# Optimization experiments

Measured on AMD Instinct MI355X. Metric: run time of the kernel, lower is better.

## Reference

```python
import jax, jax.numpy as jnp
import numpy as np

N = 50000      # nodes
E = 800000     # edges
FIN = 128      # num_feature
EDIM = 16      # edge_dim
OUT = 64       # out_dim (per-head channels; concat=False averages heads)
H = 4          # heads
SCALE = 1.0 / float(np.sqrt(OUT))


def _layernorm(h, g, b):
    mu = h.mean(-1, keepdims=True)
    var = ((h - mu) ** 2).mean(-1, keepdims=True)
    return (h - mu) * jax.lax.rsqrt(var + 1e-5) * g + b


def _tconv(x, src, dst, ea, Wq, bq, Wk, bk, Wv, bv, We, Ws, bs):
    # PyG TransformerConv, concat=False, root_weight=True, eval mode (no dropout)
    n = x.shape[0]
    q = (x @ Wq + bq).reshape(n, H, OUT)[dst]   # [E,H,D] query at destination
    k = (x @ Wk + bk).reshape(n, H, OUT)[src]   # [E,H,D] key at source
    v = (x @ Wv + bv).reshape(n, H, OUT)[src]   # [E,H,D] value at source
    e = (ea @ We).reshape(-1, H, OUT)           # [E,H,D] edge embedding (no bias)
    logits = jnp.einsum('ehd,ehd->eh', q, k + e) * SCALE   # [E,H]
    # segment softmax over incoming edges of each destination node
    m = jax.lax.stop_gradient(jax.ops.segment_max(logits, dst, num_segments=n))
    a = jnp.exp(logits - m[dst])
    s = jax.ops.segment_sum(a, dst, num_segments=n)
    alpha = a / s[dst]                                     # [E,H]
    agg = jax.ops.segment_sum((v + e) * alpha[..., None], dst, num_segments=n)  # [N,H,D]
    return agg.mean(axis=1) + x @ Ws + bs      # concat=False -> head mean; + skip


def _forward(x, src, dst, ea, p1, p2, p3, g, b):
    h = x
    for p in (p1, p2, p3):
        h = jax.nn.gelu(_layernorm(_tconv(h, src, dst, ea, *p), g, b), approximate=False)
    return h


def setup_inputs() -> dict:
    key = jax.random.key(0)
    ks = iter(jax.random.split(key, 64))
    def nrm(shp, s=0.05):
        return jax.random.normal(next(ks), shp, jnp.float32) * s
    inp = {
        'x': nrm((N, FIN), 1.0),
        'edge_index': jax.random.randint(next(ks), (2, E), 0, N),
        'edge_attr': nrm((E, EDIM), 1.0),
    }
    for l, fin in ((1, FIN), (2, OUT), (3, OUT)):
        inp[f'Wq{l}'] = nrm((fin, H * OUT)); inp[f'bq{l}'] = jnp.zeros((H * OUT,), jnp.float32)
        inp[f'Wk{l}'] = nrm((fin, H * OUT)); inp[f'bk{l}'] = jnp.zeros((H * OUT,), jnp.float32)
        inp[f'Wv{l}'] = nrm((fin, H * OUT)); inp[f'bv{l}'] = jnp.zeros((H * OUT,), jnp.float32)
        inp[f'We{l}'] = nrm((EDIM, H * OUT))
        inp[f'Ws{l}'] = nrm((fin, OUT)); inp[f'bs{l}'] = jnp.zeros((OUT,), jnp.float32)
    inp['ln_g'] = jnp.ones((OUT,), jnp.float32)
    inp['ln_b'] = jnp.zeros((OUT,), jnp.float32)
    return inp


def reference(x, edge_index, edge_attr,
              Wq1, bq1, Wk1, bk1, Wv1, bv1, We1, Ws1, bs1,
              Wq2, bq2, Wk2, bk2, Wv2, bv2, We2, Ws2, bs2,
              Wq3, bq3, Wk3, bk3, Wv3, bv3, We3, Ws3, bs3,
              ln_g, ln_b):
    src, dst = edge_index[0], edge_index[1]
    p1 = (Wq1, bq1, Wk1, bk1, Wv1, bv1, We1, Ws1, bs1)
    p2 = (Wq2, bq2, Wk2, bk2, Wv2, bv2, We2, Ws2, bs2)
    p3 = (Wq3, bq3, Wk3, bk3, Wv3, bv3, We3, Ws3, bs3)
    return _forward(x, src, dst, edge_attr, p1, p2, p3, ln_g, ln_b)
```

## Files before the change

kernel.cpp:

```cpp
#include <hip/hip_runtime.h>
#include <hip/hip_bf16.h>
#include <math.h>

#define NNODES 50000
#define NEDGES 800000
#define HD     256
#define CW     384
#define NTOT   896
#define QS     0.18033688011112042f

typedef __hip_bfloat16 bf16;
typedef unsigned short u16;
typedef unsigned char  u8;
typedef unsigned int   u32;
typedef __attribute__((ext_vector_type(8))) short bf16x8;
typedef __attribute__((ext_vector_type(4))) float f32x4;
typedef __attribute__((ext_vector_type(2))) float f32x2;

__device__ __forceinline__ float lo16f(u32 u) { return __uint_as_float(u << 16); }
__device__ __forceinline__ float hi16f(u32 u) { return __uint_as_float(u & 0xFFFF0000u); }
__device__ __forceinline__ short f2s(float v) { __hip_bfloat16 h = __float2bfloat16(v); return *(short*)&h; }

template<int CTRL>
__device__ __forceinline__ float dppadd(float x) {
    int t = __builtin_amdgcn_update_dpp(0, __float_as_int(x), CTRL, 0xF, 0xF, true);
    return x + __int_as_float(t);
}

__global__ void hist_kernel(const int* __restrict__ dst, int* __restrict__ deg, int E) {
    int e = blockIdx.x * 256 + threadIdx.x;
    if (e < E) atomicAdd(&deg[dst[e]], 1);
}

__global__ void scanA(const int* __restrict__ deg, int* __restrict__ locincl,
                      int* __restrict__ blocksum, int n) {
    int tid = threadIdx.x;
    int i = blockIdx.x * 256 + tid;
    int v = (i < n) ? deg[i] : 0;
    int lane = tid & 63, w = tid >> 6;
    int s = v;
    #pragma unroll
    for (int off = 1; off < 64; off <<= 1) {
        int t = __shfl_up(s, off);
        if (lane >= off) s += t;
    }
    __shared__ int wsum[4];
    if (lane == 63) wsum[w] = s;
    __syncthreads();
    for (int ww = 0; ww < w; ww++) s += wsum[ww];
    if (i < n) locincl[i] = s;
    if (tid == 255) blocksum[blockIdx.x] = s;
}

__global__ void scanB(const int* __restrict__ blocksum, int* __restrict__ blockoff,
                      int nb, int* __restrict__ rowptr, int n) {
    int tid = threadIdx.x;
    int v = (tid < nb) ? blocksum[tid] : 0;
    int lane = tid & 63, w = tid >> 6;
    int s = v;
    #pragma unroll
    for (int off = 1; off < 64; off <<= 1) {
        int t = __shfl_up(s, off);
        if (lane >= off) s += t;
    }
    __shared__ int wsum[4];
    if (lane == 63) wsum[w] = s;
    __syncthreads();
    for (int ww = 0; ww < w; ww++) s += wsum[ww];
    if (tid < nb) blockoff[tid] = s - v;
    if (tid == 255) rowptr[n] = s;
}

__global__ void scanC(const int* __restrict__ deg, const int* __restrict__ locincl,
                      const int* __restrict__ blockoff,
                      int* __restrict__ rowptr, int* __restrict__ cursor, int n) {
    int i = blockIdx.x * 256 + threadIdx.x;
    if (i < n) {
        int ex = locincl[i] - deg[i] + blockoff[blockIdx.x];
        rowptr[i] = ex;
        cursor[i] = ex;
    }
}

__global__ void scatter_kernel(const int* __restrict__ src, const int* __restrict__ dst,
                               int* __restrict__ cursor, int2* __restrict__ csr2, int E) {
    int e = blockIdx.x * 256 + threadIdx.x;
    if (e < E) {
        int d = dst[e];
        int p = atomicAdd(&cursor[d], 1);
        csr2[p] = make_int2(src[e], e);
    }
}

__global__ void xcast(const float* __restrict__ x, u16* __restrict__ xb) {
    int i = blockIdx.x * 256 + threadIdx.x;
    const float4* p = (const float4*)(x + (size_t)i * 8);
    float4 a = p[0], b = p[1];
    union { u16 s[8]; uint4 u; } t;
    t.s[0] = (u16)f2s(a.x); t.s[1] = (u16)f2s(a.y); t.s[2] = (u16)f2s(a.z); t.s[3] = (u16)f2s(a.w);
    t.s[4] = (u16)f2s(b.x); t.s[5] = (u16)f2s(b.y); t.s[6] = (u16)f2s(b.z); t.s[7] = (u16)f2s(b.w);
    *(uint4*)(xb + (size_t)i * 8) = t.u;
}

__global__ void pack_all(const float* __restrict__ Wq, const float* __restrict__ bq,
                         const float* __restrict__ Wk, const float* __restrict__ bk,
                         const float* __restrict__ Wv, const float* __restrict__ bv,
                         const float* __restrict__ We,
                         const float* __restrict__ Ws, const float* __restrict__ bs,
                         bf16* __restrict__ Wc, float* __restrict__ b, int K) {
    int n = blockIdx.x, c = threadIdx.x;
    float v, bb;
    if (n < 256)      { v = Wq[(size_t)c * 256 + n] * QS;    bb = bq[n] * QS; }
    else if (n < 320) {
        int t = n - 256, h = t >> 4, j = t & 15;
        float s = 0.f, sb = 0.f;
        #pragma unroll 8
        for (int d = 0; d < 64; d++) {
            float wv = We[j * HD + h * 64 + d];
            s += Wq[(size_t)c * 256 + h * 64 + d] * wv;
            sb += bq[h * 64 + d] * wv;
        }
        v = s * QS; bb = sb * QS;
    }
    else if (n < 384) { v = Ws[(size_t)c * 64  + (n - 320)]; bb = bs[n - 320]; }
    else if (n < 640) { v = Wv[(size_t)c * 256 + (n - 384)]; bb = bv[n - 384]; }
    else              { v = Wk[(size_t)c * 256 + (n - 640)]; bb = bk[n - 640]; }
    Wc[(size_t)n * K + c] = __float2bfloat16(v);
    if (c == 0) b[n] = bb;
}

template<int K>
__global__ void __launch_bounds__(256) gemm_reg(
    const u16* __restrict__ A, const bf16* __restrict__ Wc, const float* __restrict__ bias,
    bf16* __restrict__ comb, bf16* __restrict__ vbuf, u8* __restrict__ k8)
{
    constexpr int KS = K / 32;
    constexpr int ITERS = 8;
    __shared__ u8 TrB[4][2560];
    int tid = threadIdx.x, w = tid >> 6, lane = tid & 63;
    int cl = lane & 15, aq = lane >> 4;
    int chunk = blockIdx.x;
    int slab = blockIdx.y * (64 * ITERS);
    int mrow = slab + w * 16 + cl;
    u8* myT = TrB[w];

    bf16x8 bfr[4][KS];
    #pragma unroll
    for (int t = 0; t < 4; t++)
        #pragma unroll
        for (int ks = 0; ks < KS; ks++)
            bfr[t][ks] = *(const bf16x8*)((const u16*)Wc +
                         (size_t)(chunk * 64 + t * 16 + cl) * K + ks * 32 + aq * 8);

    float4 bv[4];
    #pragma unroll
    for (int t = 0; t < 4; t++) bv[t] = *(const float4*)&bias[chunk * 64 + t * 16 + aq * 4];

    auto LOADA = [&](bf16x8* af, int m) {
        int rc = (m < NNODES) ? m : (NNODES - 1);
        const u16* ar = A + (size_t)rc * K + aq * 8;
        #pragma unroll
        for (int ks = 0; ks < KS; ks++) af[ks] = *(const bf16x8*)(ar + ks * 32);
    };

    bf16x8 b0[KS], b1[KS], b2[KS];
    LOADA(b0, mrow);
    LOADA(b1, mrow + 64);
    #pragma unroll
    for (int it = 0; it < ITERS; it++) {
        int m = mrow + it * 64;
        if (it + 2 < ITERS) LOADA(b2, m + 128);
        f32x4 acc[4] = {};
        #pragma unroll
        for (int t = 0; t < 4; t++)
            #pragma unroll
            for (int ks = 0; ks < KS; ks++)
                acc[t] = __builtin_amdgcn_mfma_f32_16x16x32_bf16(bfr[t][ks], b0[ks], acc[t], 0, 0, 0);

        if (chunk < 10) {
            #pragma unroll
            for (int t = 0; t < 4; t++) {
                u32 lo = (u32)(u16)f2s(acc[t][0] + bv[t].x) | ((u32)(u16)f2s(acc[t][1] + bv[t].y) << 16);
                u32 hi = (u32)(u16)f2s(acc[t][2] + bv[t].z) | ((u32)(u16)f2s(acc[t][3] + bv[t].w) << 16);
                *(uint2*)(myT + cl * 160 + t * 32 + aq * 8) = make_uint2(lo, hi);
            }
            #pragma unroll
            for (int i = 0; i < 2; i++) {
                int r = i * 8 + (lane >> 3);
                uint4 vv = *(const uint4*)(myT + r * 160 + (lane & 7) * 16);
                int gr = slab + it * 64 + w * 16 + r;
                if (gr < NNODES) {
                    u16* dst = (chunk < 6) ? (u16*)comb + (size_t)gr * CW + chunk * 64
                                           : (u16*)vbuf + (size_t)gr * 256 + (chunk - 6) * 64;
                    *(uint4*)(dst + (lane & 7) * 8) = vv;
                }
            }
        } else {
            #pragma unroll
            for (int t = 0; t < 4; t++) {
                u32 pk = __builtin_amdgcn_cvt_pk_fp8_f32(acc[t][0] + bv[t].x, acc[t][1] + bv[t].y, 0, false);
                pk = __builtin_amdgcn_cvt_pk_fp8_f32(acc[t][2] + bv[t].z, acc[t][3] + bv[t].w, pk, true);
                *(u32*)(myT + cl * 80 + (t * 4 + aq) * 4) = pk;
            }
            {
                int r = lane >> 2;
                uint4 vv = *(const uint4*)(myT + r * 80 + (lane & 3) * 16);
                int gr = slab + it * 64 + w * 16 + r;
                if (gr < NNODES)
                    *(uint4*)(k8 + (size_t)gr * 256 + (chunk - 10) * 64 + (lane & 3) * 16) = vv;
            }
        }
        #pragma unroll
        for (int ks = 0; ks < KS; ks++) { b0[ks] = b1[ks]; b1[ks] = b2[ks]; }
    }
}

__global__ void __launch_bounds__(256) node_fused(
    const int* __restrict__ rowptr, const int2* __restrict__ csr2,
    const float* __restrict__ eattr, const u16* __restrict__ comb,
    const u16* __restrict__ vbuf, const u8* __restrict__ k8,
    const float* __restrict__ We, const float* __restrict__ lng, const float* __restrict__ lnb,
    bf16* __restrict__ outB, float* __restrict__ outF)
{
    int tid = threadIdx.x, w = tid >> 6, lane = tid & 63;
    int n = blockIdx.x * 4 + w;
    int hg = lane >> 4, j16 = lane & 15, coff = 4 * lane;
    __shared__ float sAV[4][256];
    __shared__ float sAE[4][64];

    const u16* crow = comb + (size_t)n * CW;
    uint2 qv = *(const uint2*)(crow + coff);
    float qf0 = lo16f(qv.x), qf1 = hi16f(qv.x), qf2 = lo16f(qv.y), qf3 = hi16f(qv.y);
    float qwe_r = __uint_as_float((u32)crow[256 + lane] << 16);

    int e0 = __builtin_amdgcn_readfirstlane(rowptr[n]);
    int e1 = __builtin_amdgcn_readfirstlane(rowptr[n + 1]);

    float ss = 0.f, av0 = 0.f, av1 = 0.f, av2 = 0.f, av3 = 0.f, ae = 0.f;
    u32 vo = (u32)coff * 2u;
    u32 eo = (u32)j16 * 4u;

    auto EDGE = [&](int2 me) {
        u32 s   = (u32)__builtin_amdgcn_readfirstlane(me.x);
        u32 eid = (u32)__builtin_amdgcn_readfirstlane(me.y);
        const char* kp = (const char*)k8    + ((size_t)s << 8);
        const char* vp = (const char*)vbuf  + ((size_t)s << 9);
        const char* ep = (const char*)eattr + ((size_t)eid << 6);
        u32   kw = *(const u32*)  (kp + coff);
        uint2 vw = *(const uint2*)(vp + vo);
        float ea = *(const float*)(ep + eo);
        f32x2 k01 = __builtin_amdgcn_cvt_pk_f32_fp8(kw, false);
        f32x2 k23 = __builtin_amdgcn_cvt_pk_f32_fp8(kw, true);
        float part = qf0 * k01[0] + qf1 * k01[1] + qf2 * k23[0] + qf3 * k23[1] + qwe_r * ea;
        part = dppadd<0xB1>(part);
        part = dppadd<0x4E>(part);
        part = dppadd<0x141>(part);
        part = dppadd<0x140>(part);
        float alpha = __builtin_amdgcn_exp2f(part);
        ss += alpha;
        ae += alpha * ea;
        av0 += alpha * lo16f(vw.x); av1 += alpha * hi16f(vw.x);
        av2 += alpha * lo16f(vw.y); av3 += alpha * hi16f(vw.y);
    };

    int i = e0;
    int2 c0 = make_int2(0, 0), c1 = c0, c2 = c0, c3 = c0;
    if (i + 3 < e1) { c0 = csr2[i]; c1 = csr2[i + 1]; c2 = csr2[i + 2]; c3 = csr2[i + 3]; }
    for (; i + 7 < e1; i += 4) {
        int2 p0 = csr2[i + 4], p1 = csr2[i + 5], p2 = csr2[i + 6], p3 = csr2[i + 7];
        EDGE(c0); EDGE(c1); EDGE(c2); EDGE(c3);
        c0 = p0; c1 = p1; c2 = p2; c3 = p3;
    }
    if (i + 3 < e1) { EDGE(c0); EDGE(c1); EDGE(c2); EDGE(c3); i += 4; }
    for (; i < e1; ++i) { int2 cc = csr2[i]; EDGE(cc); }

    float inv = (ss > 0.f) ? 1.f / ss : 0.f;
    *(float4*)&sAV[w][coff] = make_float4(av0 * inv, av1 * inv, av2 * inv, av3 * inv);
    sAE[w][lane] = ae * inv;

    int d = lane;
    float val = 0.f;
    #pragma unroll
    for (int h = 0; h < 4; h++) {
        float xv = sAV[w][h * 64 + d];
        #pragma unroll
        for (int j = 0; j < 16; j++) xv += sAE[w][h * 16 + j] * We[j * HD + h * 64 + d];
        val += xv;
    }
    val = val * 0.25f + __uint_as_float((u32)crow[320 + d] << 16);

    float m = val;
    #pragma unroll
    for (int off = 1; off < 64; off <<= 1) m += __shfl_xor(m, off);
    m *= (1.f / 64.f);
    float diff = val - m;
    float vr = diff * diff;
    #pragma unroll
    for (int off = 1; off < 64; off <<= 1) vr += __shfl_xor(vr, off);
    vr *= (1.f / 64.f);
    float y = diff * rsqrtf(vr + 1e-5f) * lng[d] + lnb[d];
    float ge = 0.5f * y * (1.f + erff(y * 0.70710678118654752f));
    if (outF) outF[(size_t)n * 64 + d] = ge;
    else      outB[(size_t)n * 64 + d] = __float2bfloat16(ge);
}

extern "C" void kernel_launch(void* const* d_in, const int* in_sizes, int n_in,
                              void* d_out, int out_size, void* d_ws, size_t ws_size,
                              hipStream_t stream)
{
    const float* x     = (const float*)d_in[0];
    const int*   eidx  = (const int*)d_in[1];
    const float* eattr = (const float*)d_in[2];
    struct P { const float *Wq,*bq,*Wk,*bk,*Wv,*bv,*We,*Ws,*bs; };
    P p[3];
    for (int l = 0; l < 3; l++) {
        int base = 3 + l * 9;
        p[l].Wq = (const float*)d_in[base + 0]; p[l].bq = (const float*)d_in[base + 1];
        p[l].Wk = (const float*)d_in[base + 2]; p[l].bk = (const float*)d_in[base + 3];
        p[l].Wv = (const float*)d_in[base + 4]; p[l].bv = (const float*)d_in[base + 5];
        p[l].We = (const float*)d_in[base + 6];
        p[l].Ws = (const float*)d_in[base + 7]; p[l].bs = (const float*)d_in[base + 8];
    }
    const float* lng = (const float*)d_in[30];
    const float* lnb = (const float*)d_in[31];

    char* ws = (char*)d_ws;
    size_t off = 0;
    auto alloc = [&](size_t bytes) { void* pp = ws + off; off += (bytes + 255) & ~(size_t)255; return pp; };
    int*   rowptr   = (int*)  alloc((NNODES + 1) * 4);
    int*   cursor   = (int*)  alloc(NNODES * 4);
    int*   deg      = (int*)  alloc(NNODES * 4);
    int*   blocksum = (int*)  alloc(256 * 4);
    int*   blockoff = (int*)  alloc(256 * 4);
    int2*  csr2     = (int2*) alloc((size_t)NEDGES * 8);
    bf16*  hbuf     = (bf16*) alloc((size_t)NNODES * 64 * 2);
    u16*   xb       = (u16*)  alloc((size_t)NNODES * 128 * 2);
    bf16*  comb     = (bf16*) alloc((size_t)NNODES * CW * 2);
    bf16*  vbuf     = (bf16*) alloc((size_t)NNODES * 256 * 2);
    u8*    k8       = (u8*)   alloc((size_t)NNODES * 256);
    bf16*  Wc       = (bf16*) alloc((size_t)NTOT * 128 * 2);
    float* b896     = (float*)alloc(NTOT * 4);
    (void)ws_size;

    const int* srcArr = eidx;
    const int* dstArr = eidx + NEDGES;

    int NB = (NNODES + 255) / 256;
    (void)hipMemsetAsync(deg, 0, NNODES * 4, stream);
    hist_kernel<<<(NEDGES + 255) / 256, 256, 0, stream>>>(dstArr, deg, NEDGES);
    scanA<<<NB, 256, 0, stream>>>(deg, cursor, blocksum, NNODES);
    scanB<<<1, 256, 0, stream>>>(blocksum, blockoff, NB, rowptr, NNODES);
    scanC<<<NB, 256, 0, stream>>>(deg, cursor, blockoff, rowptr, cursor, NNODES);
    scatter_kernel<<<(NEDGES + 255) / 256, 256, 0, stream>>>(srcArr, dstArr, cursor, csr2, NEDGES);
    xcast<<<(NNODES * 128 / 8 + 255) / 256, 256, 0, stream>>>(x, xb);

    int NBY = (NNODES + 511) / 512;
    int fins[3] = {128, 64, 64};

    const u16* hin = xb;
    for (int l = 0; l < 3; l++) {
        int FIN = fins[l];
        pack_all<<<NTOT, FIN, 0, stream>>>(p[l].Wq, p[l].bq, p[l].Wk, p[l].bk,
                                           p[l].Wv, p[l].bv, p[l].We, p[l].Ws, p[l].bs,
                                           Wc, b896, FIN);
        if (l == 0) gemm_reg<128><<<dim3(14, NBY), 256, 0, stream>>>(hin, Wc, b896, comb, vbuf, k8);
        else        gemm_reg<64> <<<dim3(14, NBY), 256, 0, stream>>>(hin, Wc, b896, comb, vbuf, k8);
        node_fused<<<NNODES / 4, 256, 0, stream>>>(rowptr, csr2, eattr, (const u16*)comb,
            (const u16*)vbuf, k8, p[l].We, lng, lnb,
            (l == 2) ? nullptr : hbuf, (l == 2) ? (float*)d_out : nullptr);
        hin = (const u16*)hbuf;
    }
}
```

Baseline: 655.2 us.

## Stage GEMM A tiles into swizzled double-buffered LDS via direct global-to-LDS loads

The projection GEMM stops loading A-row fragments straight into registers with a three-deep register prefetch. It now copies each 64-row A tile into a double-buffered LDS area using global_load_lds, with an XOR swizzle to avoid bank conflicts, and reads the MFMA operands back from LDS. Rows per block drop from 512 to 256 and the grid's y dimension doubles, giving more blocks for latency hiding. The cost is extra LDS use and a block-wide barrier on every iteration. The change also relies on the async LDS loads being waited on correctly before each barrier.

```diff
diff --git a/kernel.cpp b/kernel.cpp
--- a/kernel.cpp
+++ b/kernel.cpp
@@ -20,6 +20,12 @@
 __device__ __forceinline__ float lo16f(u32 u) { return __uint_as_float(u << 16); }
 __device__ __forceinline__ float hi16f(u32 u) { return __uint_as_float(u & 0xFFFF0000u); }
 __device__ __forceinline__ short f2s(float v) { __hip_bfloat16 h = __float2bfloat16(v); return *(short*)&h; }
+
+__device__ __forceinline__ void gload_lds16(const void* g, void* l) {
+    __builtin_amdgcn_global_load_lds(
+        (const __attribute__((address_space(1))) void*)g,
+        (__attribute__((address_space(3))) void*)l, 16, 0, 0);
+}
 
 template<int CTRL>
 __device__ __forceinline__ float dppadd(float x) {
@@ -130,18 +136,22 @@
 }
 
 template<int K>
-__global__ void __launch_bounds__(256) gemm_reg(
+__global__ void __launch_bounds__(256) gemm_v4(
     const u16* __restrict__ A, const bf16* __restrict__ Wc, const float* __restrict__ bias,
     bf16* __restrict__ comb, bf16* __restrict__ vbuf, u8* __restrict__ k8)
 {
-    constexpr int KS = K / 32;
-    constexpr int ITERS = 8;
-    __shared__ u8 TrB[4][2560];
+    constexpr int KS    = K / 32;
+    constexpr int ITERS = 4;
+    constexpr int ROWB  = K * 2;
+    constexpr int TILEB = 64 * ROWB;
+    constexpr int WSEG  = TILEB / 4;
+    constexpr int NINST = WSEG / 1024;
+    __shared__ __align__(16) u8 Ab[2][TILEB];
+    __shared__ __align__(16) u8 TrB[4][2560];
     int tid = threadIdx.x, w = tid >> 6, lane = tid & 63;
     int cl = lane & 15, aq = lane >> 4;
     int chunk = blockIdx.x;
     int slab = blockIdx.y * (64 * ITERS);
-    int mrow = slab + w * 16 + cl;
     u8* myT = TrB[w];
 
     bf16x8 bfr[4][KS];
@@ -156,26 +166,40 @@
     #pragma unroll
     for (int t = 0; t < 4; t++) bv[t] = *(const float4*)&bias[chunk * 64 + t * 16 + aq * 4];
 
-    auto LOADA = [&](bf16x8* af, int m) {
-        int rc = (m < NNODES) ? m : (NNODES - 1);
-        const u16* ar = A + (size_t)rc * K + aq * 8;
-        #pragma unroll
-        for (int ks = 0; ks < KS; ks++) af[ks] = *(const bf16x8*)(ar + ks * 32);
+    auto STAGE = [&](int b, int it) {
+        int m0 = slab + it * 64;
+        #pragma unroll
+        for (int i = 0; i < NINST; i++) {
+            int off = w * WSEG + i * 1024;
+            int rowbase = off / ROWB;
+            int row, gran;
+            if constexpr (K == 64) { row = rowbase + (lane >> 3); gran = lane & 7;  }
+            else                   { row = rowbase + (lane >> 4); gran = lane & 15; }
+            int gr = m0 + row; if (gr >= NNODES) gr = NNODES - 1;
+            int sg = gran ^ (row & 7);
+            gload_lds16((const u8*)A + (size_t)gr * ROWB + sg * 16, Ab[b] + off);
+        }
     };
 
-    bf16x8 b0[KS], b1[KS], b2[KS];
-    LOADA(b0, mrow);
-    LOADA(b1, mrow + 64);
+    STAGE(0, 0);
+    __syncthreads();
+    int cur = 0;
     #pragma unroll
     for (int it = 0; it < ITERS; it++) {
-        int m = mrow + it * 64;
-        if (it + 2 < ITERS) LOADA(b2, m + 128);
+        if (it + 1 < ITERS) STAGE(cur ^ 1, it + 1);
+
+        int rowt = w * 16 + cl;
+        bf16x8 a[KS];
+        #pragma unroll
+        for (int ks = 0; ks < KS; ks++)
+            a[ks] = *(const bf16x8*)&Ab[cur][rowt * ROWB + (((ks * 4 + aq) ^ (rowt & 7)) << 4)];
+
         f32x4 acc[4] = {};
         #pragma unroll
         for (int t = 0; t < 4; t++)
             #pragma unroll
             for (int ks = 0; ks < KS; ks++)
-                acc[t] = __builtin_amdgcn_mfma_f32_16x16x32_bf16(bfr[t][ks], b0[ks], acc[t], 0, 0, 0);
+                acc[t] = __builtin_amdgcn_mfma_f32_16x16x32_bf16(bfr[t][ks], a[ks], acc[t], 0, 0, 0);
 
         if (chunk < 10) {
             #pragma unroll
@@ -210,8 +234,8 @@
                     *(uint4*)(k8 + (size_t)gr * 256 + (chunk - 10) * 64 + (lane & 3) * 16) = vv;
             }
         }
-        #pragma unroll
-        for (int ks = 0; ks < KS; ks++) { b0[ks] = b1[ks]; b1[ks] = b2[ks]; }
+        __syncthreads();
+        cur ^= 1;
     }
 }
 
@@ -354,7 +378,7 @@
     scatter_kernel<<<(NEDGES + 255) / 256, 256, 0, stream>>>(srcArr, dstArr, cursor, csr2, NEDGES);
     xcast<<<(NNODES * 128 / 8 + 255) / 256, 256, 0, stream>>>(x, xb);
 
-    int NBY = (NNODES + 511) / 512;
+    int NBY = (NNODES + 255) / 256;
     int fins[3] = {128, 64, 64};
 
     const u16* hin = xb;
@@ -363,8 +387,8 @@
         pack_all<<<NTOT, FIN, 0, stream>>>(p[l].Wq, p[l].bq, p[l].Wk, p[l].bk,
                                            p[l].Wv, p[l].bv, p[l].We, p[l].Ws, p[l].bs,
                                            Wc, b896, FIN);
-        if (l == 0) gemm_reg<128><<<dim3(14, NBY), 256, 0, stream>>>(hin, Wc, b896, comb, vbuf, k8);
-        else        gemm_reg<64> <<<dim3(14, NBY), 256, 0, stream>>>(hin, Wc, b896, comb, vbuf, k8);
+        if (l == 0) gemm_v4<128><<<dim3(14, NBY), 256, 0, stream>>>(hin, Wc, b896, comb, vbuf, k8);
+        else        gemm_v4<64> <<<dim3(14, NBY), 256, 0, stream>>>(hin, Wc, b896, comb, vbuf, k8);
         node_fused<<<NNODES / 4, 256, 0, stream>>>(rowptr, csr2, eattr, (const u16*)comb,
             (const u16*)vbuf, k8, p[l].We, lng, lnb,
             (l == 2) ? nullptr : hbuf, (l == 2) ? (float*)d_out : nullptr);
```

Result: no change. 654.2 us (-0.2%).
